# Kernel optimization log

Hardware: AMD Instinct MI355X
Metric: run time of the kernel (lower is better)

## Reference

```python
import jax, jax.numpy as jnp
import numpy as np

LORA_SCALING = 2.0

def setup_inputs() -> dict:
    key = jax.random.key(0)
    ks = jax.random.split(key, 10)
    B, T, C, H, R, E = 4, 2048, 2048, 8192, 64, 4
    f32 = jnp.float32
    def w(k, shape, fan_in):
        return jax.random.normal(k, shape, f32) / np.float32(np.sqrt(fan_in))
    return {
        "x": jax.random.normal(ks[0], (B, T, C), f32),
        "x_prev": jax.random.normal(ks[1], (B, C), f32),
        "x_k": jax.random.uniform(ks[2], (1, 1, C), f32),
        "Router_ref": w(ks[3], (E - 1, C), C),
        "K_ref": w(ks[4], (C, H), C),          # right-multiplied: h @ K_ref
        "V_ref": w(ks[5], (H, C), H),          # right-multiplied: k @ V_ref
        "Ka": w(ks[6], (E, R, C), C),          # torch Linear layout [out,in]
        "Kb": w(ks[7], (E, H, R), R),
        "Va": w(ks[8], (E, R, H), H),
        "Vb": w(ks[9], (E, C, R), R),
        "MoETopk": 2,
        "MoECount": 4,
    }

def _moe_forward(x, x_prev, x_k, Router_ref, K_ref, V_ref, Ka, Kb, Va, Vb, MoETopk, MoECount):
    B, T, C = x.shape
    # token shift: mix each token with the previous one (x_prev seeds t=0)
    xx = jnp.concatenate([x_prev[:, None, :], x[:, :-1, :]], axis=1) - x
    h = (x + xx * x_k).reshape(-1, C)  # [N, C], N = B*T tokens
    N = h.shape[0]

    # router: expert 0 has implicit score 0, experts 1..E-1 come from Router_ref
    scores = h @ Router_ref.T                                   # [N, E-1]
    scores_all = jnp.concatenate([jnp.zeros((N, 1), h.dtype), scores], axis=-1)  # [N, E]
    if MoETopk < MoECount:
        topv, topi = jax.lax.top_k(scores_all, MoETopk)         # [N, K]
        gate = jax.nn.softmax(topv, axis=-1)
        gating_full = jnp.zeros_like(scores_all).at[
            jnp.arange(N)[:, None], topi].set(gate)             # [N, E], 0 for unselected
    else:
        gating_full = jax.nn.softmax(scores_all, axis=-1)

    # dense combine: gating weight is exactly 0 for unselected experts, so this
    # matches the original sparse dispatch + index_add math bit-for-bit in value.
    out = jnp.zeros_like(h)
    for e in range(MoECount):  # small fixed expert count
        k_e = jax.nn.relu(h @ K_ref + LORA_SCALING * (h @ Ka[e].T) @ Kb[e].T) ** 2  # [N, H]
        v_e = k_e @ V_ref + LORA_SCALING * (k_e @ Va[e].T) @ Vb[e].T                # [N, C]
        out = out + gating_full[:, e:e + 1] * v_e
    return out.reshape(B, T, C), x[:, -1, :]

def reference(x, x_prev, x_k, Router_ref, K_ref, V_ref, Ka, Kb, Va, Vb, MoETopk, MoECount):
    return _moe_forward(x, x_prev, x_k, Router_ref, K_ref, V_ref, Ka, Kb, Va, Vb,
                        int(MoETopk), int(MoECount))
```

## Files before the change

### kernel.cpp

```cpp
#include <hip/hip_runtime.h>


#define DEV_INLINE __device__ __forceinline__

typedef __attribute__((ext_vector_type(8))) short bf16x8;
typedef __attribute__((ext_vector_type(4))) float f32x4;

DEV_INLINE unsigned short f2bf(float f) {
  union { float f; unsigned int u; } v; v.f = f;
  unsigned int u = v.u;
  unsigned int r = (u + 0x7FFFu + ((u >> 16) & 1u)) >> 16;
  return (unsigned short)r;
}
DEV_INLINE float bf2f(unsigned short s) {
  union { unsigned int u; float f; } v; v.u = ((unsigned int)s) << 16;
  return v.f;
}


__global__ __launch_bounds__(256) void prep_kernel(
    const float* __restrict__ x, const float* __restrict__ x_prev,
    const float* __restrict__ x_k, unsigned short* __restrict__ h, int n0) {
  const int idx = blockIdx.x * 256 + threadIdx.x;
  const int c4 = idx & 511;
  const int gn = n0 + (idx >> 9);
  const int t  = gn & 2047;
  const int b  = gn >> 11;
  const float4 cur = ((const float4*)x)[(size_t)gn * 512 + c4];
  const float4 prv = (t == 0) ? ((const float4*)x_prev)[(b << 9) + c4]
                              : ((const float4*)x)[(size_t)gn * 512 - 512 + c4];
  const float4 k = ((const float4*)x_k)[c4];
  float hx = cur.x + (prv.x - cur.x) * k.x;
  float hy = cur.y + (prv.y - cur.y) * k.y;
  float hz = cur.z + (prv.z - cur.z) * k.z;
  float hw = cur.w + (prv.w - cur.w) * k.w;
  uint2 o;
  o.x = (unsigned int)f2bf(hx) | ((unsigned int)f2bf(hy) << 16);
  o.y = (unsigned int)f2bf(hz) | ((unsigned int)f2bf(hw) << 16);
  ((uint2*)h)[idx] = o;
}

__global__ __launch_bounds__(256) void xlast_kernel(
    const float* __restrict__ x, float* __restrict__ x_last) {
  const int i = blockIdx.x * 256 + threadIdx.x;
  const int b = i >> 9, c4 = i & 511;
  ((float4*)x_last)[i] =
      ((const float4*)x)[((size_t)b * 2048 + 2047) * 512 + c4];
}

__global__ __launch_bounds__(256) void transpose_cast(
    const float* __restrict__ in, unsigned short* __restrict__ outp,
    int rows, int cols) {
  __shared__ float tile[32][33];
  const int bx = blockIdx.x * 32, by = blockIdx.y * 32;
  const int tx = threadIdx.x, ty = threadIdx.y;
#pragma unroll
  for (int k = 0; k < 4; ++k)
    tile[ty + k * 8][tx] = in[(size_t)(by + ty + k * 8) * cols + bx + tx];
  __syncthreads();
#pragma unroll
  for (int k = 0; k < 4; ++k)
    outp[(size_t)(bx + ty + k * 8) * rows + by + tx] = f2bf(tile[tx][ty + k * 8]);
}

__global__ __launch_bounds__(256) void cast_bf16(
    const float* __restrict__ in, unsigned short* __restrict__ outp, int n4) {
  const int i = blockIdx.x * 256 + threadIdx.x;
  if (i >= n4) return;
  const float4 v = ((const float4*)in)[i];
  uint2 o;
  o.x = (unsigned int)f2bf(v.x) | ((unsigned int)f2bf(v.y) << 16);
  o.y = (unsigned int)f2bf(v.z) | ((unsigned int)f2bf(v.w) << 16);
  ((uint2*)outp)[i] = o;
}

__global__ void zero_page(unsigned int* zp) {
  if (threadIdx.x < 64) zp[threadIdx.x] = 0;
}

__global__ __launch_bounds__(256) void router_kernel(
    const float* __restrict__ x, const float* __restrict__ x_prev,
    const float* __restrict__ x_k, const float* __restrict__ Rt,
    int* __restrict__ tbl, int* __restrict__ etok,
    float* __restrict__ gate_tok, int MC, int n0) {
  const int lane = threadIdx.x & 63, wid = threadIdx.x >> 6;
  const int nl = blockIdx.x * 4 + wid;
  const int gn = n0 + nl;
  const int t = gn & 2047, b = gn >> 11;
  const float* cur = x + (size_t)gn * 2048;
  const float* prv = (t == 0) ? x_prev + (size_t)b * 2048 : cur - 2048;
  float hv[32];
#pragma unroll
  for (int j = 0; j < 32; ++j) {
    const int i = j * 64 + lane;
    const float xc = cur[i];
    hv[j] = xc + (prv[i] - xc) * x_k[i];
  }
  float s[4];
  s[0] = 0.f;
  for (int e = 1; e < 4; ++e) {
    const float* rrow = Rt + (size_t)(e - 1) * 2048;
    float a = 0.f;
#pragma unroll
    for (int j = 0; j < 32; ++j) a += hv[j] * rrow[j * 64 + lane];
#pragma unroll
    for (int d = 32; d >= 1; d >>= 1) a += __shfl_xor(a, d, 64);
    s[e] = a;
  }
  if (lane == 0) {
    int i1 = 0; float v1 = s[0];
    for (int e = 1; e < 4; ++e) if (s[e] > v1) { v1 = s[e]; i1 = e; }
    int i2 = -1; float v2 = -1e30f;
    for (int e = 0; e < 4; ++e) if (e != i1 && s[e] > v2) { v2 = s[e]; i2 = e; }
    const float ex = expf(v2 - v1);
    const float g1 = 1.f / (1.f + ex), g2 = ex / (1.f + ex);
    etok[nl] = i1;          etok[MC + nl] = i2;
    gate_tok[nl] = g1;      gate_tok[MC + nl] = g2;
    atomicAdd(&tbl[i1], 1); atomicAdd(&tbl[4 + i2], 1);
  }
}

__global__ void zero_hist(int* tbl) {
  if (threadIdx.x < 8) tbl[threadIdx.x] = 0;
}

__global__ __launch_bounds__(128) void seg_build(int* __restrict__ tbl, int MB) {
  const int tid = threadIdx.x;
  __shared__ int sbase[2][5];
  if (tid == 0) {
    for (int k = 0; k < 2; ++k) {
      int b = 0; sbase[k][0] = 0;
      for (int e = 0; e < 4; ++e) {
        b += ((tbl[k * 4 + e] + 127) >> 7) << 7;
        sbase[k][e + 1] = b;
      }
      for (int e = 0; e < 5; ++e) tbl[16 + k * 5 + e] = sbase[k][e];
    }
    for (int i = 0; i < 8; ++i) tbl[8 + i] = 0;
  }
  __syncthreads();
  int* bt = tbl + 32;
  for (int i = tid; i < 2 * MB; i += 128) {
    const int k = i / MB, row = (i % MB) * 128;
    int e = -1;
    for (int q = 0; q < 4; ++q)
      if (row >= sbase[k][q] && row < sbase[k][q + 1]) e = q;
    bt[i] = e;
  }
  int* tok = tbl + 32 + 2 * MB;
  for (int i = tid; i < 2 * MB * 128; i += 128) tok[i] = -1;
}

__global__ __launch_bounds__(256) void scatter_build(
    int* __restrict__ tbl, const int* __restrict__ etok, int MC, int MB) {
  const int t = blockIdx.x * 256 + threadIdx.x;
  if (t >= MC) return;
  int* tok = tbl + 32 + 2 * MB;
#pragma unroll
  for (int k = 0; k < 2; ++k) {
    const int e = etok[k * MC + t];
    const int r = atomicAdd(&tbl[8 + k * 4 + e], 1);
    tok[k * MB * 128 + tbl[16 + k * 5 + e] + r] = t;
  }
}

__global__ __launch_bounds__(512, 1) void gemm256(
    const unsigned short* __restrict__ A, int lda,
    const unsigned short* __restrict__ Bt, int ldb,
    unsigned short* __restrict__ C, int ldc, int K, int nbx) {
  __shared__ char smem[2][2][256 * 64 * 2];
  const int nwg = gridDim.x, wg = blockIdx.x;
  const int q = nwg >> 3, r = nwg & 7;
  const int xcd = wg & 7, loc = wg >> 3;
  const int swz = (xcd < r ? xcd * (q + 1) : r * (q + 1) + (xcd - r) * q) + loc;
  const int bx = swz % nbx, by = swz / nbx;
  const int m0 = by * 256, n0 = bx * 256;
  const int tid = threadIdx.x, lane = tid & 63;
  const int wid = tid >> 6, wr = wid >> 2, wc = wid & 3;

  int arow[4], scol[4];
#pragma unroll
  for (int i = 0; i < 4; ++i) {
    const int qq = i * 512 + tid;
    const int row = qq >> 3, w = qq & 7;
    arow[i] = row;
    scol[i] = (w ^ (row & 7)) * 8;
  }

  f32x4 acc[8][4] = {};

  auto stage = [&](int buf, int kt) {
#pragma unroll
    for (int i = 0; i < 4; ++i) {
      const unsigned short* src =
          A + (size_t)(m0 + arow[i]) * lda + kt + scol[i];
      __builtin_amdgcn_global_load_lds(
          (const __attribute__((address_space(1))) void*)src,
          (__attribute__((address_space(3))) void*)(
              &smem[buf][0][(i * 512 + tid) * 16]), 16, 0, 0);
    }
#pragma unroll
    for (int i = 0; i < 4; ++i) {
      const unsigned short* src =
          Bt + (size_t)(n0 + arow[i]) * ldb + kt + scol[i];
      __builtin_amdgcn_global_load_lds(
          (const __attribute__((address_space(1))) void*)src,
          (__attribute__((address_space(3))) void*)(
              &smem[buf][1][(i * 512 + tid) * 16]), 16, 0, 0);
    }
  };

  stage(0, 0);
  asm volatile("s_waitcnt vmcnt(0)" ::: "memory");
  __syncthreads();

  const int NT = K >> 6;
  for (int t = 0; t < NT; ++t) {
    const int cur = t & 1;
    if (t + 1 < NT) stage(cur ^ 1, (t + 1) << 6);
    const char* As = smem[cur][0];
    const char* Bs = smem[cur][1];
#pragma unroll
    for (int ks = 0; ks < 2; ++ks) {
#pragma unroll
      for (int mh = 0; mh < 2; ++mh) {
        bf16x8 af[4];
#pragma unroll
        for (int m = 0; m < 4; ++m) {
          const int row = wr * 128 + mh * 64 + m * 16 + (lane & 15);
          const int kb = (ks * 64 + ((lane >> 4) * 16)) ^ ((row & 7) << 4);
          af[m] = *(const bf16x8*)(As + row * 128 + kb);
        }
#pragma unroll
        for (int nh = 0; nh < 2; ++nh) {
          bf16x8 bf[2];
#pragma unroll
          for (int n = 0; n < 2; ++n) {
            const int row = wc * 64 + nh * 32 + n * 16 + (lane & 15);
            const int kb = (ks * 64 + ((lane >> 4) * 16)) ^ ((row & 7) << 4);
            bf[n] = *(const bf16x8*)(Bs + row * 128 + kb);
          }
          __builtin_amdgcn_s_setprio(1);
#pragma unroll
          for (int m = 0; m < 4; ++m)
#pragma unroll
            for (int n = 0; n < 2; ++n)
              acc[mh * 4 + m][nh * 2 + n] =
                  __builtin_amdgcn_mfma_f32_16x16x32_bf16(
                      af[m], bf[n], acc[mh * 4 + m][nh * 2 + n], 0, 0, 0);
          __builtin_amdgcn_s_setprio(0);
        }
      }
    }
    asm volatile("s_waitcnt vmcnt(0)" ::: "memory");
    __syncthreads();
  }

  const int cc = lane & 15, cr0 = (lane >> 4) * 4;
#pragma unroll
  for (int mf = 0; mf < 8; ++mf)
#pragma unroll
    for (int nf = 0; nf < 4; ++nf)
#pragma unroll
      for (int j = 0; j < 4; ++j) {
        const int grow = m0 + wr * 128 + mf * 16 + cr0 + j;
        const int gcol = n0 + wc * 64 + nf * 16 + cc;
        C[(size_t)grow * ldc + gcol] = f2bf(acc[mf][nf][j]);
      }
}

enum { EPI_BF16 = 0, EPI_KE = 1, EPI_GV = 2, EPI_VB0 = 3, EPI_VB1 = 4 };

template <int EPI>
__global__ __launch_bounds__(256) void gemm_bt(
    const unsigned short* __restrict__ A, int lda, long long strideAe,
    long long strideAslot,
    const unsigned short* __restrict__ B, int ldb, long long strideBe,
    const unsigned short* __restrict__ B2, const unsigned short* __restrict__ zp,
    void* __restrict__ Cp, int ldc, long long strideCslot,
    unsigned short* __restrict__ vatp, long long strideVat,
    const unsigned short* __restrict__ aux, int ldaux,
    const float* __restrict__ gate, const float* __restrict__ out2,
    float scale,
    const int* __restrict__ blocktab, const int* __restrict__ rowmap,
    const int* __restrict__ crowmap,
    int K, int nbx, int mbPerSlot, int PRr, int MCr) {
  constexpr int BM = 128, BN = 128, BK = 64;

  const int nwg = gridDim.x, wg = blockIdx.x;
  const int q = nwg >> 3, r = nwg & 7;
  const int xcd = wg & 7, loc = wg >> 3;
  const int swz = (xcd < r ? xcd * (q + 1) : r * (q + 1) + (xcd - r) * q) + loc;
  const int bx = swz % nbx;
  const int by = swz / nbx;

  int k = 0, byl = by;
  if (mbPerSlot > 0) { k = by / mbPerSlot; byl = by - k * mbPerSlot; }

  int e = 0;
  if (blocktab) { e = blocktab[by]; if (e < 0) return; }

  __shared__ alignas(16) char smem[(BM + BN) * BK * 2];
  char* As = smem;
  char* Bs = smem + BM * BK * 2;

  const unsigned short* Ae = A + (size_t)e * strideAe + (size_t)k * strideAslot;
  const bool vatBlk = (EPI == EPI_GV) && (B2 != nullptr) && (bx == nbx - 1);

  const int tid = threadIdx.x;
  const int lane = tid & 63;
  const int wid = tid >> 6;
  const int wr = wid >> 1, wc = wid & 1;
  const int m0 = byl * BM;
  const int bn0 = bx * BN;

  const int* tokA = rowmap ? rowmap + k * PRr : nullptr;
  int arow[4];
#pragma unroll
  for (int i = 0; i < 4; ++i) {
    const int row = (i * 256 + tid) >> 3;
    int rr = m0 + row;
    if (tokA) { rr = tokA[rr]; if (rr < 0) rr = 0; }
    arow[i] = rr;
  }

  f32x4 acc[4][4] = {};

  for (int kt = 0; kt < K; kt += BK) {
    __syncthreads();
#pragma unroll
    for (int i = 0; i < 4; ++i) {
      const int qq = i * 256 + tid;
      const int row = qq >> 3, w = qq & 7;
      const int g = w ^ (row & 7);
      const unsigned short* src = Ae + (size_t)arow[i] * lda + kt + g * 8;
      __builtin_amdgcn_global_load_lds(
          (const __attribute__((address_space(1))) void*)src,
          (__attribute__((address_space(3))) void*)(As + qq * 16), 16, 0, 0);
    }
#pragma unroll
    for (int i = 0; i < 4; ++i) {
      const int qq = i * 256 + tid;
      const int row = qq >> 3, w = qq & 7;
      const int g = w ^ (row & 7);
      const unsigned short* src;
      if (vatBlk) {
        src = (row < 64) ? B2 + ((size_t)e * 64 + row) * ldb + kt + g * 8
                         : (const unsigned short*)zp;
      } else {
        src = B + (size_t)e * strideBe + (size_t)(bn0 + row) * ldb + kt + g * 8;
      }
      __builtin_amdgcn_global_load_lds(
          (const __attribute__((address_space(1))) void*)src,
          (__attribute__((address_space(3))) void*)(Bs + qq * 16), 16, 0, 0);
    }
    asm volatile("s_waitcnt vmcnt(0)" ::: "memory");
    __syncthreads();

#pragma unroll
    for (int ks = 0; ks < 2; ++ks) {
      bf16x8 af[4], bfr[4];
#pragma unroll
      for (int m = 0; m < 4; ++m) {
        const int row = wr * 64 + m * 16 + (lane & 15);
        const int kb = (ks * 64 + ((lane >> 4) * 16)) ^ ((row & 7) << 4);
        af[m] = *(const bf16x8*)(As + row * 128 + kb);
      }
#pragma unroll
      for (int n = 0; n < 4; ++n) {
        const int row = wc * 64 + n * 16 + (lane & 15);
        const int kb = (ks * 64 + ((lane >> 4) * 16)) ^ ((row & 7) << 4);
        bfr[n] = *(const bf16x8*)(Bs + row * 128 + kb);
      }
#pragma unroll
      for (int m = 0; m < 4; ++m)
#pragma unroll
        for (int n = 0; n < 4; ++n)
          acc[m][n] = __builtin_amdgcn_mfma_f32_16x16x32_bf16(
              af[m], bfr[n], acc[m][n], 0, 0, 0);
    }
  }

  const int cc = lane & 15;
  const int cr0 = (lane >> 4) * 4;
#pragma unroll
  for (int m = 0; m < 4; ++m) {
#pragma unroll
    for (int n = 0; n < 4; ++n) {
#pragma unroll
      for (int j = 0; j < 4; ++j) {
        const int grow = m0 + wr * 64 + m * 16 + cr0 + j;
        const int lcol = wc * 64 + n * 16 + cc;
        const float v = acc[m][n][j];
        if constexpr (EPI == EPI_BF16) {
          ((unsigned short*)Cp)[(size_t)grow * ldc + bn0 + lcol] = f2bf(v);
        } else if constexpr (EPI == EPI_KE) {
          int ar = grow;
          if (tokA) { ar = tokA[grow]; if (ar < 0) ar = 0; }
          const float ksv = bf2f(aux[(size_t)ar * ldaux + bn0 + lcol]);
          float rr = ksv + 2.0f * v;
          rr = rr > 0.f ? rr : 0.f;
          ((unsigned short*)Cp + (size_t)k * strideCslot)
              [(size_t)grow * ldc + bn0 + lcol] = f2bf(rr * rr);
        } else if constexpr (EPI == EPI_GV) {
          if (vatBlk) {
            if (lcol < 64)
              (vatp + (size_t)k * strideVat)[(size_t)grow * 64 + lcol] = f2bf(v);
          } else {
            const int t = crowmap[k * PRr + grow];
            if (t >= 0) {
              const float g = gate[k * MCr + t] * scale;
              ((float*)Cp + (size_t)k * strideCslot)[(size_t)t * ldc + bn0 + lcol] =
                  g * v;
            }
          }
        } else if constexpr (EPI == EPI_VB0) {
          const int t = crowmap[grow];
          if (t >= 0) {
            const float g = gate[t] * scale;
            float* o = (float*)Cp + (size_t)t * ldc + bn0 + lcol;
            *o = *o + g * v;
          }
        } else {
          const int t = crowmap[grow];
          if (t >= 0) {
            const float g = gate[t] * scale;
            float* o = (float*)Cp + (size_t)t * ldc + bn0 + lcol;
            *o = *o + out2[(size_t)t * ldc + bn0 + lcol] + g * v;
          }
        }
      }
    }
  }
}

extern "C" void kernel_launch(void* const* d_in, const int* in_sizes, int n_in,
                              void* d_out, int out_size, void* d_ws,
                              size_t ws_size, hipStream_t stream) {
  (void)in_sizes; (void)n_in; (void)out_size;
  const float* x      = (const float*)d_in[0];
  const float* x_prev = (const float*)d_in[1];
  const float* x_k    = (const float*)d_in[2];
  const float* Router = (const float*)d_in[3];
  const float* K_ref  = (const float*)d_in[4];
  const float* V_ref  = (const float*)d_in[5];
  const float* Ka     = (const float*)d_in[6];
  const float* Kb     = (const float*)d_in[7];
  const float* Va     = (const float*)d_in[8];
  const float* Vb     = (const float*)d_in[9];

  constexpr int Bb = 4, T = 2048, C = 2048, H = 8192, R = 64, E = 4;
  constexpr int M = Bb * T;

  const size_t PAD = 255;
  auto rnd = [&](size_t b) { return (b + PAD) & ~PAD; };
  const size_t persist = rnd((size_t)H * C * 2) + rnd((size_t)C * H * 2)
                       + rnd((size_t)E * R * C * 2) + rnd((size_t)E * H * R * 2)
                       + rnd((size_t)E * R * H * 2) + rnd((size_t)E * C * R * 2)
                       + rnd(256);

  int MC = 0;
  for (int cand = M; cand >= 2048; cand >>= 1) {
    const int mb = cand / 128 + 4;
    const size_t per = rnd((size_t)cand * C * 2)
                     + rnd((size_t)cand * E * R * 2)
                     + rnd((size_t)cand * H * 2)
                     + rnd((size_t)2 * mb * 128 * H * 2)
                     + rnd((size_t)2 * mb * 128 * 64 * 2)
                     + rnd((size_t)cand * C * 4)
                     + rnd((size_t)(32 + 2 * mb + 2 * mb * 128) * 4)
                     + rnd((size_t)2 * cand * 4)
                     + rnd((size_t)2 * cand * 4);
    if (persist + per <= ws_size) { MC = cand; break; }
  }
  if (MC == 0) return;
  const int MB = MC / 128 + 4;
  const int PR = MB * 128;

  char* ws = (char*)d_ws;
  size_t off = 0;
  auto alloc = [&](size_t bytes) -> char* {
    char* p = ws + off; off += rnd(bytes); return p;
  };
  unsigned short* Kt   = (unsigned short*)alloc((size_t)H * C * 2);
  unsigned short* Vt   = (unsigned short*)alloc((size_t)C * H * 2);
  unsigned short* KaB  = (unsigned short*)alloc((size_t)E * R * C * 2);
  unsigned short* KbB  = (unsigned short*)alloc((size_t)E * H * R * 2);
  unsigned short* VaB  = (unsigned short*)alloc((size_t)E * R * H * 2);
  unsigned short* VbB  = (unsigned short*)alloc((size_t)E * C * R * 2);
  unsigned short* zp   = (unsigned short*)alloc(256);
  unsigned short* h_c  = (unsigned short*)alloc((size_t)MC * C * 2);
  unsigned short* lora = (unsigned short*)alloc((size_t)MC * E * R * 2);
  unsigned short* ksh  = (unsigned short*)alloc((size_t)MC * H * 2);
  unsigned short* k_e  = (unsigned short*)alloc((size_t)2 * PR * H * 2);
  unsigned short* vat  = (unsigned short*)alloc((size_t)2 * PR * 64 * 2);
  float*          out2 = (float*)alloc((size_t)MC * C * 4);
  int*            tbl  = (int*)alloc((size_t)(32 + 2 * MB + 2 * PR) * 4);
  int*            etok = (int*)alloc((size_t)2 * MC * 4);
  float*          gtok = (float*)alloc((size_t)2 * MC * 4);

  float* out    = (float*)d_out;
  float* x_last = out + (size_t)M * C;

  transpose_cast<<<dim3(H / 32, C / 32), dim3(32, 8), 0, stream>>>(K_ref, Kt, C, H);
  transpose_cast<<<dim3(C / 32, H / 32), dim3(32, 8), 0, stream>>>(V_ref, Vt, H, C);
  cast_bf16<<<(E * R * C / 4 + 255) / 256, 256, 0, stream>>>(Ka, KaB, E * R * C / 4);
  cast_bf16<<<(E * H * R / 4 + 255) / 256, 256, 0, stream>>>(Kb, KbB, E * H * R / 4);
  cast_bf16<<<(E * R * H / 4 + 255) / 256, 256, 0, stream>>>(Va, VaB, E * R * H / 4);
  cast_bf16<<<(E * C * R / 4 + 255) / 256, 256, 0, stream>>>(Vb, VbB, E * C * R / 4);
  zero_page<<<1, 64, 0, stream>>>((unsigned int*)zp);
  xlast_kernel<<<Bb * C / 4 / 256, 256, 0, stream>>>(x, x_last);

  for (int c0 = 0; c0 < M; c0 += MC) {
    float* outc = out + (size_t)c0 * C;
    prep_kernel<<<MC * C / 4 / 256, 256, 0, stream>>>(x, x_prev, x_k, h_c, c0);
    zero_hist<<<1, 64, 0, stream>>>(tbl);
    router_kernel<<<MC / 4, 256, 0, stream>>>(x, x_prev, x_k, Router, tbl,
                                              etok, gtok, MC, c0);
    seg_build<<<1, 128, 0, stream>>>(tbl, MB);
    scatter_build<<<(MC + 255) / 256, 256, 0, stream>>>(tbl, etok, MC, MB);

    const int* bt  = tbl + 32;
    const int* tok = tbl + 32 + 2 * MB;

    gemm256<<<(MC / 256) * (H / 256), 512, 0, stream>>>(
        h_c, C, Kt, C, ksh, H, C, H / 256);

    gemm_bt<EPI_BF16><<<(E * R / 128) * (MC / 128), 256, 0, stream>>>(
        h_c, C, 0, 0, KaB, C, 0, nullptr, nullptr, lora, E * R, 0,
        nullptr, 0, nullptr, 0, nullptr, nullptr, 0.f,
        nullptr, nullptr, nullptr, C, E * R / 128, 0, PR, MC);

    gemm_bt<EPI_KE><<<(H / 128) * 2 * MB, 256, 0, stream>>>(
        lora, E * R, R, 0, KbB, R, (long long)H * R, nullptr, nullptr,
        k_e, H, (long long)PR * H, nullptr, 0, ksh, H, nullptr, nullptr, 0.f,
        bt, tok, nullptr, R, H / 128, MB, PR, MC);

    gemm_bt<EPI_GV><<<(C / 128 + 1) * 2 * MB, 256, 0, stream>>>(
        k_e, H, 0, (long long)PR * H, Vt, H, 0, VaB, zp,
        outc, C, (long long)(out2 - outc), vat, (long long)PR * 64,
        nullptr, 0, gtok, nullptr, 1.0f,
        bt, nullptr, tok, H, C / 128 + 1, MB, PR, MC);

    gemm_bt<EPI_VB0><<<(C / 128) * MB, 256, 0, stream>>>(
        vat, 64, 0, 0, VbB, R, (long long)C * R, nullptr, nullptr,
        outc, C, 0, nullptr, 0, nullptr, 0, gtok, nullptr, 2.0f,
        bt, nullptr, tok, R, C / 128, 0, PR, MC);

    gemm_bt<EPI_VB1><<<(C / 128) * MB, 256, 0, stream>>>(
        vat + (size_t)PR * 64, 64, 0, 0, VbB, R, (long long)C * R,
        nullptr, nullptr, outc, C, 0, nullptr, 0, nullptr, 0,
        gtok + MC, out2, 2.0f,
        bt + MB, nullptr, tok + PR, R, C / 128, 0, PR, MC);
  }
}
```

Baseline: 2.317 ms.

## Fuse LoRA-A projections into big 256-tile GEMMs and reuse workspace buffers

```diff
diff --git a/kernel.cpp b/kernel.cpp
--- a/kernel.cpp
+++ b/kernel.cpp
@@ -74,10 +74,6 @@
   ((uint2*)outp)[i] = o;
 }
 
-__global__ void zero_page(unsigned int* zp) {
-  if (threadIdx.x < 64) zp[threadIdx.x] = 0;
-}
-
 __global__ __launch_bounds__(256) void router_kernel(
     const float* __restrict__ x, const float* __restrict__ x_prev,
     const float* __restrict__ x_k, const float* __restrict__ Rt,
@@ -164,10 +160,16 @@
   }
 }
 
+enum { EPI256_D = 0, EPI256_OUT = 1 };
+
+template <int EPI>
 __global__ __launch_bounds__(512, 1) void gemm256(
     const unsigned short* __restrict__ A, int lda,
     const unsigned short* __restrict__ Bt, int ldb,
-    unsigned short* __restrict__ C, int ldc, int K, int nbx) {
+    void* __restrict__ Cp, int ldc, int K, int nbx,
+    const int* __restrict__ tok, const int* __restrict__ etok,
+    const float* __restrict__ gtok, unsigned short* __restrict__ out2,
+    unsigned short* __restrict__ vatp, int PRr, int MCr) {
   __shared__ char smem[2][2][256 * 64 * 2];
   const int nwg = gridDim.x, wg = blockIdx.x;
   const int q = nwg >> 3, r = nwg & 7;
@@ -258,29 +260,46 @@
 
   const int cc = lane & 15, cr0 = (lane >> 4) * 4;
 #pragma unroll
-  for (int mf = 0; mf < 8; ++mf)
-#pragma unroll
-    for (int nf = 0; nf < 4; ++nf)
+  for (int mf = 0; mf < 8; ++mf) {
+#pragma unroll
+    for (int nf = 0; nf < 4; ++nf) {
 #pragma unroll
       for (int j = 0; j < 4; ++j) {
         const int grow = m0 + wr * 128 + mf * 16 + cr0 + j;
-        const int gcol = n0 + wc * 64 + nf * 16 + cc;
-        C[(size_t)grow * ldc + gcol] = f2bf(acc[mf][nf][j]);
+        const int lcol = wc * 64 + nf * 16 + cc;
+        const float v = acc[mf][nf][j];
+        if constexpr (EPI == EPI256_D) {
+          ((unsigned short*)Cp)[(size_t)grow * ldc + n0 + lcol] = f2bf(v);
+        } else {
+          const int t = tok[grow];
+          if (t >= 0) {
+            const int k = (grow >= PRr) ? 1 : 0;
+            if (bx == nbx - 1) {
+              const int e = etok[k * MCr + t];
+              if ((lcol >> 6) == e)
+                vatp[(size_t)grow * 64 + (lcol & 63)] = f2bf(v);
+            } else {
+              const float g = gtok[k * MCr + t];
+              const int gc = bx * 256 + lcol;
+              if (k == 0) ((float*)Cp)[(size_t)t * ldc + gc] = g * v;
+              else        out2[(size_t)t * ldc + gc] = f2bf(g * v);
+            }
+          }
+        }
       }
-}
-
-enum { EPI_BF16 = 0, EPI_KE = 1, EPI_GV = 2, EPI_VB0 = 3, EPI_VB1 = 4 };
+    }
+  }
+}
+
+enum { EPI_KE = 0, EPI_VB0 = 1, EPI_VB1 = 2 };
 
 template <int EPI>
 __global__ __launch_bounds__(256) void gemm_bt(
     const unsigned short* __restrict__ A, int lda, long long strideAe,
-    long long strideAslot,
     const unsigned short* __restrict__ B, int ldb, long long strideBe,
-    const unsigned short* __restrict__ B2, const unsigned short* __restrict__ zp,
     void* __restrict__ Cp, int ldc, long long strideCslot,
-    unsigned short* __restrict__ vatp, long long strideVat,
     const unsigned short* __restrict__ aux, int ldaux,
-    const float* __restrict__ gate, const float* __restrict__ out2,
+    const float* __restrict__ gate, const unsigned short* __restrict__ out2,
     float scale,
     const int* __restrict__ blocktab, const int* __restrict__ rowmap,
     const int* __restrict__ crowmap,
@@ -304,8 +323,7 @@
   char* As = smem;
   char* Bs = smem + BM * BK * 2;
 
-  const unsigned short* Ae = A + (size_t)e * strideAe + (size_t)k * strideAslot;
-  const bool vatBlk = (EPI == EPI_GV) && (B2 != nullptr) && (bx == nbx - 1);
+  const unsigned short* Ae = A + (size_t)e * strideAe;
 
   const int tid = threadIdx.x;
   const int lane = tid & 63;
@@ -343,13 +361,8 @@
       const int qq = i * 256 + tid;
       const int row = qq >> 3, w = qq & 7;
       const int g = w ^ (row & 7);
-      const unsigned short* src;
-      if (vatBlk) {
-        src = (row < 64) ? B2 + ((size_t)e * 64 + row) * ldb + kt + g * 8
-                         : (const unsigned short*)zp;
-      } else {
-        src = B + (size_t)e * strideBe + (size_t)(bn0 + row) * ldb + kt + g * 8;
-      }
+      const unsigned short* src =
+          B + (size_t)e * strideBe + (size_t)(bn0 + row) * ldb + kt + g * 8;
       __builtin_amdgcn_global_load_lds(
           (const __attribute__((address_space(1))) void*)src,
           (__attribute__((address_space(3))) void*)(Bs + qq * 16), 16, 0, 0);
@@ -392,9 +405,7 @@
         const int grow = m0 + wr * 64 + m * 16 + cr0 + j;
         const int lcol = wc * 64 + n * 16 + cc;
         const float v = acc[m][n][j];
-        if constexpr (EPI == EPI_BF16) {
-          ((unsigned short*)Cp)[(size_t)grow * ldc + bn0 + lcol] = f2bf(v);
-        } else if constexpr (EPI == EPI_KE) {
+        if constexpr (EPI == EPI_KE) {
           int ar = grow;
           if (tokA) { ar = tokA[grow]; if (ar < 0) ar = 0; }
           const float ksv = bf2f(aux[(size_t)ar * ldaux + bn0 + lcol]);
@@ -402,18 +413,6 @@
           rr = rr > 0.f ? rr : 0.f;
           ((unsigned short*)Cp + (size_t)k * strideCslot)
               [(size_t)grow * ldc + bn0 + lcol] = f2bf(rr * rr);
-        } else if constexpr (EPI == EPI_GV) {
-          if (vatBlk) {
-            if (lcol < 64)
-              (vatp + (size_t)k * strideVat)[(size_t)grow * 64 + lcol] = f2bf(v);
-          } else {
-            const int t = crowmap[k * PRr + grow];
-            if (t >= 0) {
-              const float g = gate[k * MCr + t] * scale;
-              ((float*)Cp + (size_t)k * strideCslot)[(size_t)t * ldc + bn0 + lcol] =
-                  g * v;
-            }
-          }
         } else if constexpr (EPI == EPI_VB0) {
           const int t = crowmap[grow];
           if (t >= 0) {
@@ -426,7 +425,7 @@
           if (t >= 0) {
             const float g = gate[t] * scale;
             float* o = (float*)Cp + (size_t)t * ldc + bn0 + lcol;
-            *o = *o + out2[(size_t)t * ldc + bn0 + lcol] + g * v;
+            *o = *o + bf2f(out2[(size_t)t * ldc + bn0 + lcol]) + g * v;
           }
         }
       }
@@ -451,27 +450,26 @@
 
   constexpr int Bb = 4, T = 2048, C = 2048, H = 8192, R = 64, E = 4;
   constexpr int M = Bb * T;
+  constexpr int NKL = H + E * R;
+  constexpr int NVV = C + E * R;
 
   const size_t PAD = 255;
   auto rnd = [&](size_t b) { return (b + PAD) & ~PAD; };
-  const size_t persist = rnd((size_t)H * C * 2) + rnd((size_t)C * H * 2)
-                       + rnd((size_t)E * R * C * 2) + rnd((size_t)E * H * R * 2)
-                       + rnd((size_t)E * R * H * 2) + rnd((size_t)E * C * R * 2)
-                       + rnd(256);
+  const size_t persist = rnd((size_t)NKL * C * 2)
+                       + rnd((size_t)NVV * H * 2)
+                       + rnd((size_t)E * H * R * 2)
+                       + rnd((size_t)E * C * R * 2);
 
   int MC = 0;
-  for (int cand = M; cand >= 2048; cand >>= 1) {
+  for (int cand = M; cand >= 1024; cand >>= 1) {
     const int mb = cand / 128 + 4;
-    const size_t per = rnd((size_t)cand * C * 2)
-                     + rnd((size_t)cand * E * R * 2)
-                     + rnd((size_t)cand * H * 2)
-                     + rnd((size_t)2 * mb * 128 * H * 2)
-                     + rnd((size_t)2 * mb * 128 * 64 * 2)
-                     + rnd((size_t)cand * C * 4)
-                     + rnd((size_t)(32 + 2 * mb + 2 * mb * 128) * 4)
-                     + rnd((size_t)2 * cand * 4)
-                     + rnd((size_t)2 * cand * 4);
-    if (persist + per <= ws_size) { MC = cand; break; }
+    const long long pr = (long long)mb * 128;
+    const size_t span0 = rnd((size_t)2 * pr * H * 2);
+    const size_t span1 = rnd((size_t)cand * NKL * 2);
+    const size_t rest = rnd((size_t)2 * pr * 64 * 2)
+                      + rnd((size_t)(32 + 2 * mb + 2 * pr) * 4)
+                      + rnd((size_t)2 * cand * 4) + rnd((size_t)2 * cand * 4);
+    if (persist + span0 + span1 + rest <= ws_size) { MC = cand; break; }
   }
   if (MC == 0) return;
   const int MB = MC / 128 + 4;
@@ -482,33 +480,30 @@
   auto alloc = [&](size_t bytes) -> char* {
     char* p = ws + off; off += rnd(bytes); return p;
   };
-  unsigned short* Kt   = (unsigned short*)alloc((size_t)H * C * 2);
-  unsigned short* Vt   = (unsigned short*)alloc((size_t)C * H * 2);
-  unsigned short* KaB  = (unsigned short*)alloc((size_t)E * R * C * 2);
+  unsigned short* KtKa = (unsigned short*)alloc((size_t)NKL * C * 2);
+  unsigned short* VtVa = (unsigned short*)alloc((size_t)NVV * H * 2);
   unsigned short* KbB  = (unsigned short*)alloc((size_t)E * H * R * 2);
-  unsigned short* VaB  = (unsigned short*)alloc((size_t)E * R * H * 2);
   unsigned short* VbB  = (unsigned short*)alloc((size_t)E * C * R * 2);
-  unsigned short* zp   = (unsigned short*)alloc(256);
-  unsigned short* h_c  = (unsigned short*)alloc((size_t)MC * C * 2);
-  unsigned short* lora = (unsigned short*)alloc((size_t)MC * E * R * 2);
-  unsigned short* ksh  = (unsigned short*)alloc((size_t)MC * H * 2);
   unsigned short* k_e  = (unsigned short*)alloc((size_t)2 * PR * H * 2);
+  unsigned short* ksl  = (unsigned short*)alloc((size_t)MC * NKL * 2);
   unsigned short* vat  = (unsigned short*)alloc((size_t)2 * PR * 64 * 2);
-  float*          out2 = (float*)alloc((size_t)MC * C * 4);
   int*            tbl  = (int*)alloc((size_t)(32 + 2 * MB + 2 * PR) * 4);
   int*            etok = (int*)alloc((size_t)2 * MC * 4);
   float*          gtok = (float*)alloc((size_t)2 * MC * 4);
+  unsigned short* h_c  = k_e;
+  unsigned short* out2 = ksl;
 
   float* out    = (float*)d_out;
   float* x_last = out + (size_t)M * C;
 
-  transpose_cast<<<dim3(H / 32, C / 32), dim3(32, 8), 0, stream>>>(K_ref, Kt, C, H);
-  transpose_cast<<<dim3(C / 32, H / 32), dim3(32, 8), 0, stream>>>(V_ref, Vt, H, C);
-  cast_bf16<<<(E * R * C / 4 + 255) / 256, 256, 0, stream>>>(Ka, KaB, E * R * C / 4);
+  transpose_cast<<<dim3(H / 32, C / 32), dim3(32, 8), 0, stream>>>(K_ref, KtKa, C, H);
+  cast_bf16<<<(E * R * C / 4 + 255) / 256, 256, 0, stream>>>(
+      Ka, KtKa + (size_t)H * C, E * R * C / 4);
+  transpose_cast<<<dim3(C / 32, H / 32), dim3(32, 8), 0, stream>>>(V_ref, VtVa, H, C);
+  cast_bf16<<<(E * R * H / 4 + 255) / 256, 256, 0, stream>>>(
+      Va, VtVa + (size_t)C * H, E * R * H / 4);
   cast_bf16<<<(E * H * R / 4 + 255) / 256, 256, 0, stream>>>(Kb, KbB, E * H * R / 4);
-  cast_bf16<<<(E * R * H / 4 + 255) / 256, 256, 0, stream>>>(Va, VaB, E * R * H / 4);
   cast_bf16<<<(E * C * R / 4 + 255) / 256, 256, 0, stream>>>(Vb, VbB, E * C * R / 4);
-  zero_page<<<1, 64, 0, stream>>>((unsigned int*)zp);
   xlast_kernel<<<Bb * C / 4 / 256, 256, 0, stream>>>(x, x_last);
 
   for (int c0 = 0; c0 < M; c0 += MC) {
@@ -523,34 +518,27 @@
     const int* bt  = tbl + 32;
     const int* tok = tbl + 32 + 2 * MB;
 
-    gemm256<<<(MC / 256) * (H / 256), 512, 0, stream>>>(
-        h_c, C, Kt, C, ksh, H, C, H / 256);
-
-    gemm_bt<EPI_BF16><<<(E * R / 128) * (MC / 128), 256, 0, stream>>>(
-        h_c, C, 0, 0, KaB, C, 0, nullptr, nullptr, lora, E * R, 0,
-        nullptr, 0, nullptr, 0, nullptr, nullptr, 0.f,
-        nullptr, nullptr, nullptr, C, E * R / 128, 0, PR, MC);
+    gemm256<EPI256_D><<<(MC / 256) * (NKL / 256), 512, 0, stream>>>(
+        h_c, C, KtKa, C, ksl, NKL, C, NKL / 256,
+        nullptr, nullptr, nullptr, nullptr, nullptr, PR, MC);
 
     gemm_bt<EPI_KE><<<(H / 128) * 2 * MB, 256, 0, stream>>>(
-        lora, E * R, R, 0, KbB, R, (long long)H * R, nullptr, nullptr,
-        k_e, H, (long long)PR * H, nullptr, 0, ksh, H, nullptr, nullptr, 0.f,
+        ksl + H, NKL, 64, KbB, R, (long long)H * R,
+        k_e, H, (long long)PR * H, ksl, NKL, nullptr, nullptr, 0.f,
         bt, tok, nullptr, R, H / 128, MB, PR, MC);
 
-    gemm_bt<EPI_GV><<<(C / 128 + 1) * 2 * MB, 256, 0, stream>>>(
-        k_e, H, 0, (long long)PR * H, Vt, H, 0, VaB, zp,
-        outc, C, (long long)(out2 - outc), vat, (long long)PR * 64,
-        nullptr, 0, gtok, nullptr, 1.0f,
-        bt, nullptr, tok, H, C / 128 + 1, MB, PR, MC);
+    gemm256<EPI256_OUT><<<(2 * PR / 256) * (NVV / 256), 512, 0, stream>>>(
+        k_e, H, VtVa, H, outc, C, H, NVV / 256,
+        tok, etok, gtok, out2, vat, PR, MC);
 
     gemm_bt<EPI_VB0><<<(C / 128) * MB, 256, 0, stream>>>(
-        vat, 64, 0, 0, VbB, R, (long long)C * R, nullptr, nullptr,
-        outc, C, 0, nullptr, 0, nullptr, 0, gtok, nullptr, 2.0f,
+        vat, 64, 0, VbB, R, (long long)C * R,
+        outc, C, 0, nullptr, 0, gtok, nullptr, 2.0f,
         bt, nullptr, tok, R, C / 128, 0, PR, MC);
 
     gemm_bt<EPI_VB1><<<(C / 128) * MB, 256, 0, stream>>>(
-        vat + (size_t)PR * 64, 64, 0, 0, VbB, R, (long long)C * R,
-        nullptr, nullptr, outc, C, 0, nullptr, 0, nullptr, 0,
-        gtok + MC, out2, 2.0f,
+        vat + (size_t)PR * 64, 64, 0, VbB, R, (long long)C * R,
+        outc, C, 0, nullptr, 0, gtok + MC, out2, 2.0f,
         bt + MB, nullptr, tok + PR, R, C / 128, 0, PR, MC);
   }
 }
```

Result: slower. 2.648 ms (+14.3%).

## Process top-k slots sequentially and alias workspace buffers to enlarge token chunks

Applied to the files above, without the earlier changes.

```diff
diff --git a/kernel.cpp b/kernel.cpp
--- a/kernel.cpp
+++ b/kernel.cpp
@@ -454,24 +454,29 @@
 
   const size_t PAD = 255;
   auto rnd = [&](size_t b) { return (b + PAD) & ~PAD; };
-  const size_t persist = rnd((size_t)H * C * 2) + rnd((size_t)C * H * 2)
-                       + rnd((size_t)E * R * C * 2) + rnd((size_t)E * H * R * 2)
-                       + rnd((size_t)E * R * H * 2) + rnd((size_t)E * C * R * 2)
+  const size_t persist = rnd((size_t)H * C * 2)
+                       + rnd((size_t)C * H * 2)
+                       + rnd((size_t)E * R * C * 2)
+                       + rnd((size_t)E * H * R * 2)
+                       + rnd((size_t)E * R * H * 2)
+                       + rnd((size_t)E * C * R * 2)
                        + rnd(256);
 
   int MC = 0;
-  for (int cand = M; cand >= 2048; cand >>= 1) {
+  for (int cand = M; cand >= 1024; cand >>= 1) {
     const int mb = cand / 128 + 4;
-    const size_t per = rnd((size_t)cand * C * 2)
-                     + rnd((size_t)cand * E * R * 2)
-                     + rnd((size_t)cand * H * 2)
-                     + rnd((size_t)2 * mb * 128 * H * 2)
-                     + rnd((size_t)2 * mb * 128 * 64 * 2)
-                     + rnd((size_t)cand * C * 4)
-                     + rnd((size_t)(32 + 2 * mb + 2 * mb * 128) * 4)
-                     + rnd((size_t)2 * cand * 4)
-                     + rnd((size_t)2 * cand * 4);
-    if (persist + per <= ws_size) { MC = cand; break; }
+    const long long pr = (long long)mb * 128;
+    size_t keSpan = rnd((size_t)pr * H * 2);
+    if (keSpan < rnd((size_t)cand * C * 2)) keSpan = rnd((size_t)cand * C * 2);
+    size_t kshSpan = rnd((size_t)cand * H * 2);
+    if (kshSpan < rnd((size_t)cand * C * 4)) kshSpan = rnd((size_t)cand * C * 4);
+    const size_t need = persist + keSpan + kshSpan
+                      + rnd((size_t)cand * E * R * 2)
+                      + rnd((size_t)2 * pr * 64 * 2)
+                      + rnd((size_t)(32 + 2 * mb + 2 * pr) * 4)
+                      + rnd((size_t)2 * cand * 4)
+                      + rnd((size_t)2 * cand * 4);
+    if (need <= ws_size) { MC = cand; break; }
   }
   if (MC == 0) return;
   const int MB = MC / 128 + 4;
@@ -489,15 +494,19 @@
   unsigned short* VaB  = (unsigned short*)alloc((size_t)E * R * H * 2);
   unsigned short* VbB  = (unsigned short*)alloc((size_t)E * C * R * 2);
   unsigned short* zp   = (unsigned short*)alloc(256);
-  unsigned short* h_c  = (unsigned short*)alloc((size_t)MC * C * 2);
+  size_t keBytes = rnd((size_t)PR * H * 2);
+  if (keBytes < rnd((size_t)MC * C * 2)) keBytes = rnd((size_t)MC * C * 2);
+  unsigned short* k_e  = (unsigned short*)alloc(keBytes);
+  size_t kshBytes = rnd((size_t)MC * H * 2);
+  if (kshBytes < rnd((size_t)MC * C * 4)) kshBytes = rnd((size_t)MC * C * 4);
+  unsigned short* ksh  = (unsigned short*)alloc(kshBytes);
   unsigned short* lora = (unsigned short*)alloc((size_t)MC * E * R * 2);
-  unsigned short* ksh  = (unsigned short*)alloc((size_t)MC * H * 2);
-  unsigned short* k_e  = (unsigned short*)alloc((size_t)2 * PR * H * 2);
   unsigned short* vat  = (unsigned short*)alloc((size_t)2 * PR * 64 * 2);
-  float*          out2 = (float*)alloc((size_t)MC * C * 4);
   int*            tbl  = (int*)alloc((size_t)(32 + 2 * MB + 2 * PR) * 4);
   int*            etok = (int*)alloc((size_t)2 * MC * 4);
   float*          gtok = (float*)alloc((size_t)2 * MC * 4);
+  unsigned short* h_c  = k_e;
+  float*          out2 = (float*)ksh;
 
   float* out    = (float*)d_out;
   float* x_last = out + (size_t)M * C;
@@ -531,26 +540,34 @@
         nullptr, 0, nullptr, 0, nullptr, nullptr, 0.f,
         nullptr, nullptr, nullptr, C, E * R / 128, 0, PR, MC);
 
-    gemm_bt<EPI_KE><<<(H / 128) * 2 * MB, 256, 0, stream>>>(
-        lora, E * R, R, 0, KbB, R, (long long)H * R, nullptr, nullptr,
-        k_e, H, (long long)PR * H, nullptr, 0, ksh, H, nullptr, nullptr, 0.f,
-        bt, tok, nullptr, R, H / 128, MB, PR, MC);
-
-    gemm_bt<EPI_GV><<<(C / 128 + 1) * 2 * MB, 256, 0, stream>>>(
-        k_e, H, 0, (long long)PR * H, Vt, H, 0, VaB, zp,
-        outc, C, (long long)(out2 - outc), vat, (long long)PR * 64,
-        nullptr, 0, gtok, nullptr, 1.0f,
-        bt, nullptr, tok, H, C / 128 + 1, MB, PR, MC);
-
-    gemm_bt<EPI_VB0><<<(C / 128) * MB, 256, 0, stream>>>(
-        vat, 64, 0, 0, VbB, R, (long long)C * R, nullptr, nullptr,
-        outc, C, 0, nullptr, 0, nullptr, 0, gtok, nullptr, 2.0f,
-        bt, nullptr, tok, R, C / 128, 0, PR, MC);
-
-    gemm_bt<EPI_VB1><<<(C / 128) * MB, 256, 0, stream>>>(
-        vat + (size_t)PR * 64, 64, 0, 0, VbB, R, (long long)C * R,
-        nullptr, nullptr, outc, C, 0, nullptr, 0, nullptr, 0,
-        gtok + MC, out2, 2.0f,
-        bt + MB, nullptr, tok + PR, R, C / 128, 0, PR, MC);
-  }
-}
+    for (int k = 0; k < 2; ++k) {
+      const int* btk  = bt + k * MB;
+      const int* tokk = tok + k * PR;
+      const float* gk = gtok + (size_t)k * MC;
+
+      gemm_bt<EPI_KE><<<(H / 128) * MB, 256, 0, stream>>>(
+          lora, E * R, R, 0, KbB, R, (long long)H * R, nullptr, nullptr,
+          k_e, H, 0, nullptr, 0, ksh, H, nullptr, nullptr, 0.f,
+          btk, tokk, nullptr, R, H / 128, 0, PR, MC);
+
+      gemm_bt<EPI_GV><<<(C / 128 + 1) * MB, 256, 0, stream>>>(
+          k_e, H, 0, 0, Vt, H, 0, VaB, zp,
+          (k == 0) ? (void*)outc : (void*)out2, C, 0,
+          vat + (size_t)k * PR * 64, 0, nullptr, 0, gk, nullptr, 1.0f,
+          btk, nullptr, tokk, H, C / 128 + 1, 0, PR, MC);
+
+      if (k == 0) {
+        gemm_bt<EPI_VB0><<<(C / 128) * MB, 256, 0, stream>>>(
+            vat, 64, 0, 0, VbB, R, (long long)C * R, nullptr, nullptr,
+            outc, C, 0, nullptr, 0, nullptr, 0, gk, nullptr, 2.0f,
+            btk, nullptr, tokk, R, C / 128, 0, PR, MC);
+      } else {
+        gemm_bt<EPI_VB1><<<(C / 128) * MB, 256, 0, stream>>>(
+            vat + (size_t)PR * 64, 64, 0, 0, VbB, R, (long long)C * R,
+            nullptr, nullptr, outc, C, 0, nullptr, 0, nullptr, 0,
+            gk, out2, 2.0f,
+            btk, nullptr, tokk, R, C / 128, 0, PR, MC);
+      }
+    }
+  }
+}
```

Measured after the change: 2.027 ms. 12.5% less time.
